# Performance work log

Measured on AMD Instinct MI355X. Metric: run time of the kernel, lower is better.

The kernel has to match this reference:

```python
import jax, jax.numpy as jnp
import numpy as np

B, S, H = 2, 2048, 1024
N_HEAD = 16
HEAD_DIM = H // N_HEAD


def setup_inputs() -> dict:
    key = jax.random.key(0)
    ks = jax.random.split(key, 8)
    init = 0.02
    return {
        "hidden_states": jax.random.normal(ks[0], (B, S, H), dtype=jnp.float32),
        "residual": jax.random.normal(ks[1], (B, S, H), dtype=jnp.float32),
        "alibi": jax.random.normal(ks[2], (B * N_HEAD, 1, S), dtype=jnp.float32),
        "attention_mask": jnp.ones((B, S), dtype=bool),
        "w_qkv": jax.random.normal(ks[3], (H, 3 * H), dtype=jnp.float32) * init,
        "b_qkv": jax.random.normal(ks[4], (3 * H,), dtype=jnp.float32) * init,
        "w_o": jax.random.normal(ks[5], (H, H), dtype=jnp.float32) * init,
        "b_o": jax.random.normal(ks[6], (H,), dtype=jnp.float32) * init,
        "layer_number": 4,
    }


def reference(hidden_states, residual, alibi, attention_mask, w_qkv, b_qkv, w_o, b_o, layer_number):
    b, s, h = hidden_states.shape
    nh, hd = N_HEAD, HEAD_DIM
    # fused QKV projection: (B,S,3H) -> (B,S,nh,3*hd) -> split
    fused_qkv = (hidden_states @ w_qkv + b_qkv).reshape(b, s, nh, 3 * hd)
    query, key, value = jnp.split(fused_qkv, 3, axis=-1)  # each (B,S,nh,hd)

    L = max(int(layer_number), 1)
    alpha = 1.0 / (np.sqrt(hd).astype(np.float32) * L)
    beta = 1.0 / L

    # scores = beta*alibi + alpha * q@k^T, reshaped to (B,nh,Sq,Sk)
    scores = jnp.einsum("bqnh,bknh->bnqk", query, key) * alpha
    scores = scores + beta * alibi.reshape(b, nh, 1, s)
    # FlaxBloomScaledSoftmax applies scale = layer_number before masking
    scores = scores * L

    # fused causal + padding mask (attention_mask_func): keep = causal & pad_q & pad_k
    causal = jnp.tril(jnp.ones((s, s), dtype=bool))
    pad = attention_mask  # (B,S) bool, True = attend
    keep = causal[None, None, :, :] & pad[:, None, :, None] & pad[:, None, None, :]  # (B,1,S,S)

    masked_scores = jnp.where(keep, scores, jnp.float32(-10000.0))
    probs = jax.nn.softmax(masked_scores.astype(jnp.float32), axis=-1) * keep
    probs = probs.astype(hidden_states.dtype)

    context = jnp.einsum("bnqk,bknh->bqnh", probs, value).reshape(b, s, h)
    attn_output = context @ w_o + b_o + residual
    return attn_output
```

## Files before the change

### kernel.cpp

```cpp
#include <hip/hip_runtime.h>
#include <hip/hip_bf16.h>

#define S_LEN 2048
#define HID   1024
#define NHEAD 16
#define HDIM  64
#define NBH   32

#define QSCALE 0.18033688f
#define LOG2E  1.44269504f

typedef __attribute__((ext_vector_type(8))) short short8;
typedef __attribute__((ext_vector_type(4))) float f32x4;

__device__ inline void gload_lds16(const void* g, void* l) {
  __builtin_amdgcn_global_load_lds(
      (const __attribute__((address_space(1))) void*)g,
      (__attribute__((address_space(3))) void*)l, 16, 0, 0);
}

__device__ inline ushort f2bf(float f) {
  __hip_bfloat16 h = __float2bfloat16(f);
  return *reinterpret_cast<const ushort*>(&h);
}

__device__ inline float exp2_fast(float x) {
  float r;
  asm("v_exp_f32 %0, %1" : "=v"(r) : "v"(x));
  return r;
}

__global__ __launch_bounds__(256) void convert_bf16(
    const float* __restrict__ in, ushort* __restrict__ out, int n8)
{
    int i = blockIdx.x * 256 + threadIdx.x;
    if (i < n8) {
        float4 a = ((const float4*)in)[i * 2];
        float4 b = ((const float4*)in)[i * 2 + 1];
        union { ushort u[8]; uint4 v; } o;
        o.u[0]=f2bf(a.x); o.u[1]=f2bf(a.y); o.u[2]=f2bf(a.z); o.u[3]=f2bf(a.w);
        o.u[4]=f2bf(b.x); o.u[5]=f2bf(b.y); o.u[6]=f2bf(b.z); o.u[7]=f2bf(b.w);
        ((uint4*)out)[i] = o.v;
    }
}

__global__ __launch_bounds__(256) void transpose_convert(
    const float* __restrict__ in, ushort* __restrict__ out, int R, int C)
{
    __shared__ ushort Ls[64][72];
    const int c0 = blockIdx.x * 64, r0 = blockIdx.y * 64;
    const int t = threadIdx.x;
    const int tr = t >> 4, tc = (t & 15) * 4;
    #pragma unroll
    for (int i = 0; i < 4; ++i) {
        int gr = r0 + tr + i * 16;
        float4 v = *(const float4*)(in + (size_t)gr * C + c0 + tc);
        Ls[tc + 0][tr + i * 16] = f2bf(v.x);
        Ls[tc + 1][tr + i * 16] = f2bf(v.y);
        Ls[tc + 2][tr + i * 16] = f2bf(v.z);
        Ls[tc + 3][tr + i * 16] = f2bf(v.w);
    }
    __syncthreads();
    #pragma unroll
    for (int i = 0; i < 4; ++i) {
        int oc = c0 + tr + i * 16;
        ushort4 v = *(const ushort4*)&Ls[tr + i * 16][tc];
        *(ushort4*)(out + (size_t)oc * R + r0 + tc) = v;
    }
}

__global__ __launch_bounds__(512, 2) void qkv_gemm_mfma(
    const ushort* __restrict__ A, const ushort* __restrict__ Bt,
    const float* __restrict__ bias,
    ushort* __restrict__ Q, ushort* __restrict__ K, ushort* __restrict__ V)
{
    __shared__ __align__(16) ushort As[2][256 * 64];
    __shared__ __align__(16) ushort Bs[2][192 * 64];
    const int tid = threadIdx.x;
    const int l   = tid & 63;
    const int w   = tid >> 6;
    const int wm  = w >> 2;
    const int wn  = w & 3;
    const int l7  = l & 7, l15 = l & 15, g = l >> 4;
    const int srow = l >> 3;
    const int schunk = l7 ^ srow;

    int lin = blockIdx.y * 16 + blockIdx.x;
    int swz = (lin & 7) * 32 + (lin >> 3);
    const int m0 = (swz >> 4) * 256;
    const int n0 = (swz & 15) * 192;

    f32x4 acc[8][3];
    #pragma unroll
    for (int i = 0; i < 8; ++i)
        #pragma unroll
        for (int j = 0; j < 3; ++j) acc[i][j] = (f32x4){0.f, 0.f, 0.f, 0.f};

#define STG_A(tt, qq) gload_lds16(A + (size_t)(m0 + (qq)*64 + w*8 + srow)*1024 \
                                    + (tt)*64 + schunk*8,                      \
                                  As[(tt) & 1] + ((qq)*64 + w*8)*64)
#define STG_B(tt, qq) gload_lds16(Bt + (size_t)(n0 + (qq)*64 + w*8 + srow)*1024 \
                                    + (tt)*64 + schunk*8,                       \
                                  Bs[(tt) & 1] + ((qq)*64 + w*8)*64)
#define LD_A(bb, mf, kk) (*(const short8*)(As[bb] + ((mf)*32 + wm*16 + l15)*64 \
                                           + ((((kk)*4 + g) ^ l7) << 3)))
#define LD_B(bb, nf, kk) (*(const short8*)(Bs[bb] + (wn*48 + (nf)*16 + l15)*64 \
                                           + ((((kk)*4 + g) ^ l7) << 3)))

    #pragma unroll
    for (int qq = 0; qq < 4; ++qq) STG_A(0, qq);
    #pragma unroll
    for (int qq = 0; qq < 3; ++qq) STG_B(0, qq);
    #pragma unroll
    for (int qq = 0; qq < 3; ++qq) { STG_A(1, qq); STG_B(1, qq); }
    asm volatile("s_waitcnt vmcnt(6)" ::: "memory");
    __builtin_amdgcn_s_barrier();

    short8 bfr[6];

    for (int it = 0; it < 8; ++it) {
        const int t = 2 * it;
        #pragma unroll
        for (int ph = 0; ph < 4; ++ph) {
            short8 afr[4];
            afr[0] = LD_A(0, 2*ph,     0);
            afr[1] = LD_A(0, 2*ph,     1);
            afr[2] = LD_A(0, 2*ph + 1, 0);
            afr[3] = LD_A(0, 2*ph + 1, 1);
            if (ph == 0) {
                #pragma unroll
                for (int nf = 0; nf < 3; ++nf) {
                    bfr[nf*2 + 0] = LD_B(0, nf, 0);
                    bfr[nf*2 + 1] = LD_B(0, nf, 1);
                }
            }
            if (ph == 0) { STG_A(t + 1, 3); }
            else if (t + 2 < 16) { STG_A(t + 2, ph - 1); STG_B(t + 2, ph - 1); }
            __builtin_amdgcn_s_barrier();
            asm volatile("s_waitcnt lgkmcnt(0)" ::: "memory");
            __builtin_amdgcn_sched_barrier(0);
            __builtin_amdgcn_s_setprio(1);
            #pragma unroll
            for (int kk = 0; kk < 2; ++kk)
                #pragma unroll
                for (int mi = 0; mi < 2; ++mi)
                    #pragma unroll
                    for (int nf = 0; nf < 3; ++nf)
                        acc[2*ph + mi][nf] = __builtin_amdgcn_mfma_f32_16x16x32_bf16(
                            afr[mi*2 + kk], bfr[nf*2 + kk], acc[2*ph + mi][nf], 0, 0, 0);
            __builtin_amdgcn_s_setprio(0);
            if (ph == 3) {
                if (it == 7) asm volatile("s_waitcnt vmcnt(0)" ::: "memory");
                else         asm volatile("s_waitcnt vmcnt(6)" ::: "memory");
            }
            __builtin_amdgcn_s_barrier();
        }
        #pragma unroll
        for (int ph = 0; ph < 4; ++ph) {
            short8 afr[4];
            afr[0] = LD_A(1, 2*ph,     0);
            afr[1] = LD_A(1, 2*ph,     1);
            afr[2] = LD_A(1, 2*ph + 1, 0);
            afr[3] = LD_A(1, 2*ph + 1, 1);
            if (ph == 0) {
                #pragma unroll
                for (int nf = 0; nf < 3; ++nf) {
                    bfr[nf*2 + 0] = LD_B(1, nf, 0);
                    bfr[nf*2 + 1] = LD_B(1, nf, 1);
                }
            }
            if (ph == 0) { if (t + 2 < 16) STG_A(t + 2, 3); }
            else if (t + 3 < 16) { STG_A(t + 3, ph - 1); STG_B(t + 3, ph - 1); }
            __builtin_amdgcn_s_barrier();
            asm volatile("s_waitcnt lgkmcnt(0)" ::: "memory");
            __builtin_amdgcn_sched_barrier(0);
            __builtin_amdgcn_s_setprio(1);
            #pragma unroll
            for (int kk = 0; kk < 2; ++kk)
                #pragma unroll
                for (int mi = 0; mi < 2; ++mi)
                    #pragma unroll
                    for (int nf = 0; nf < 3; ++nf)
                        acc[2*ph + mi][nf] = __builtin_amdgcn_mfma_f32_16x16x32_bf16(
                            afr[mi*2 + kk], bfr[nf*2 + kk], acc[2*ph + mi][nf], 0, 0, 0);
            __builtin_amdgcn_s_setprio(0);
            if (ph == 3) asm volatile("s_waitcnt vmcnt(6)" ::: "memory");
            __builtin_amdgcn_s_barrier();
        }
    }
#undef STG_A
#undef STG_B
#undef LD_A
#undef LD_B

    #pragma unroll
    for (int nf = 0; nf < 3; ++nf) {
        int gcol = n0 + wn * 48 + nf * 16 + l15;
        int head = gcol / 192;
        int rem  = gcol - head * 192;
        int which = rem >> 6;
        int d     = rem & 63;
        float bv = bias[gcol];
        #pragma unroll
        for (int mf = 0; mf < 8; ++mf) {
            int grow = m0 + mf * 32 + wm * 16 + g * 4;
            int bb = grow >> 11;
            int ss = grow & 2047;
            int bhh = (bb << 4) + head;
            if (which == 2) {
                ushort4 pk;
                pk.x = f2bf(acc[mf][nf][0] + bv);
                pk.y = f2bf(acc[mf][nf][1] + bv);
                pk.z = f2bf(acc[mf][nf][2] + bv);
                pk.w = f2bf(acc[mf][nf][3] + bv);
                *(ushort4*)(V + ((size_t)bhh * 64 + d) * S_LEN + ss) = pk;
            } else {
                ushort* plane = (which == 0) ? Q : K;
                float sc = (which == 0) ? QSCALE : 1.0f;
                ushort* dst = plane + (((size_t)bhh * S_LEN + ss) << 6) + d;
                #pragma unroll
                for (int r = 0; r < 4; ++r)
                    dst[(size_t)r << 6] = f2bf((acc[mf][nf][r] + bv) * sc);
            }
        }
    }
}

#define GEMM_STAGE(A_, Bt_, kk0, buf) do {                                    \
    _Pragma("unroll")                                                         \
    for (int i = 0; i < 4; ++i) {                                             \
        int row = i * 32 + w * 8 + srow;                                      \
        gload_lds16(A_ + (size_t)(m0 + row) * 1024 + (kk0) + schunk * 8,      \
                    Asl[buf] + (i * 32 + w * 8) * 64);                        \
        gload_lds16(Bt_ + (size_t)(n0 + row) * 1024 + (kk0) + schunk * 8,     \
                    Bsl[buf] + (i * 32 + w * 8) * 64);                        \
    }                                                                         \
} while (0)

#define GEMM_CORE(A_, Bt_)                                                    \
    __shared__ ushort Asl[2][128 * 64];                                       \
    __shared__ ushort Bsl[2][128 * 64];                                       \
    const int tid = threadIdx.x;                                              \
    const int l = tid & 63;                                                   \
    const int w = tid >> 6;                                                   \
    const int wm = (w >> 1) * 64;                                             \
    const int wn = (w & 1) * 64;                                              \
    const int m0 = blockIdx.y * 128;                                          \
    const int n0 = blockIdx.x * 128;                                          \
    const int l15 = l & 15, g = l >> 4;                                       \
    const int srow = l >> 3;                                                  \
    const int schunk = (l & 7) ^ srow;                                        \
    f32x4 acc[4][4];                                                          \
    _Pragma("unroll")                                                         \
    for (int i = 0; i < 4; ++i)                                               \
        _Pragma("unroll")                                                     \
        for (int j = 0; j < 4; ++j) acc[i][j] = (f32x4){0.f, 0.f, 0.f, 0.f};  \
    GEMM_STAGE(A_, Bt_, 0, 0);                                                \
    __syncthreads();                                                          \
    for (int ks = 0; ks < 16; ++ks) {                                         \
        const int cur = ks & 1;                                               \
        if (ks < 15) GEMM_STAGE(A_, Bt_, (ks + 1) * 64, cur ^ 1);             \
        const ushort* Acur = Asl[cur];                                        \
        const ushort* Bcur = Bsl[cur];                                        \
        _Pragma("unroll")                                                     \
        for (int kk = 0; kk < 2; ++kk) {                                      \
            short8 af[4], bf[4];                                              \
            _Pragma("unroll")                                                 \
            for (int mf = 0; mf < 4; ++mf) {                                  \
                int row = wm + mf * 16 + l15;                                 \
                int ch = (kk * 4 + g) ^ (row & 7);                            \
                af[mf] = *(const short8*)(Acur + row * 64 + ch * 8);          \
            }                                                                 \
            _Pragma("unroll")                                                 \
            for (int nf = 0; nf < 4; ++nf) {                                  \
                int row = wn + nf * 16 + l15;                                 \
                int ch = (kk * 4 + g) ^ (row & 7);                            \
                bf[nf] = *(const short8*)(Bcur + row * 64 + ch * 8);          \
            }                                                                 \
            _Pragma("unroll")                                                 \
            for (int mf = 0; mf < 4; ++mf)                                    \
                _Pragma("unroll")                                             \
                for (int nf = 0; nf < 4; ++nf)                                \
                    acc[mf][nf] = __builtin_amdgcn_mfma_f32_16x16x32_bf16(    \
                        af[mf], bf[nf], acc[mf][nf], 0, 0, 0);                \
        }                                                                     \
        __syncthreads();                                                      \
    }

__global__ __launch_bounds__(256) void out_gemm_mfma(
    const ushort* __restrict__ A, const ushort* __restrict__ Bt,
    const float* __restrict__ bias, const float* __restrict__ resid,
    float* __restrict__ out)
{
    GEMM_CORE(A, Bt)
    #pragma unroll
    for (int nf = 0; nf < 4; ++nf) {
        int gcol = n0 + wn + nf * 16 + l15;
        float bv = bias[gcol];
        #pragma unroll
        for (int mf = 0; mf < 4; ++mf) {
            int grow = m0 + wm + mf * 16 + g * 4;
            #pragma unroll
            for (int r = 0; r < 4; ++r) {
                size_t idx = (size_t)(grow + r) * 1024 + gcol;
                out[idx] = acc[mf][nf][r] + bv + resid[idx];
            }
        }
    }
}

#define STAGE(tt, idx) do {                                                   \
    gload_lds16(Kbh + (size_t)((tt) * 64 + w * 8 + srow) * 64 + schunk * 8,   \
                Ks[idx] + (w * 8) * 64);                                      \
    gload_lds16(Vbh + (size_t)(w * 8 + srow) * S_LEN + (tt) * 64 + schunk * 8,\
                Vs[idx] + (w * 8) * 64);                                      \
} while (0)

#define QK_TILE(SN, tt, idx, FULL) do {                                       \
    const ushort* Kc = Ks[idx];                                               \
    _Pragma("unroll")                                                         \
    for (int kb = 0; kb < 4; ++kb) {                                          \
        float4 a4 = *(const float4*)&alib[(tt) * 64 + kb * 16 + g * 4];       \
        SN[kb] = (f32x4){a4.x, a4.y, a4.z, a4.w};                             \
        if (FULL || (tt) * 64 + kb * 16 <= qmax) {                            \
            int row = kb * 16 + l15;                                          \
            short8 ka0 = *(const short8*)(Kc + row * 64 + ((g ^ l7) << 3));   \
            short8 ka1 = *(const short8*)(Kc + row * 64 + (((4+g) ^ l7) << 3));\
            SN[kb] = __builtin_amdgcn_mfma_f32_16x16x32_bf16(ka0, qb0, SN[kb], 0, 0, 0); \
            SN[kb] = __builtin_amdgcn_mfma_f32_16x16x32_bf16(ka1, qb1, SN[kb], 0, 0, 0); \
        }                                                                     \
    }                                                                         \
} while (0)

#define SM_PV(SC, tt, idx, FULL) do {                                         \
    const ushort* Vc = Vs[idx];                                               \
    ushort* Pw = Ps[w];                                                       \
    float p[16];                                                              \
    _Pragma("unroll")                                                         \
    for (int kb = 0; kb < 4; ++kb) {                                          \
        _Pragma("unroll")                                                     \
        for (int r = 0; r < 4; ++r) {                                         \
            float s = SC[kb][r];                                              \
            if (!FULL) {                                                      \
                int kglob = (tt) * 64 + kb * 16 + g * 4 + r;                  \
                s = (kglob > qglob) ? -1e30f : s;                             \
            }                                                                 \
            p[kb * 4 + r] = s;                                                \
        }                                                                     \
    }                                                                         \
    float mx0 = fmaxf(fmaxf(p[0], p[1]),   fmaxf(p[2], p[3]));                \
    float mx1 = fmaxf(fmaxf(p[4], p[5]),   fmaxf(p[6], p[7]));                \
    float mx2 = fmaxf(fmaxf(p[8], p[9]),   fmaxf(p[10], p[11]));              \
    float mx3 = fmaxf(fmaxf(p[12], p[13]), fmaxf(p[14], p[15]));              \
    float pmax = fmaxf(fmaxf(mx0, mx1), fmaxf(mx2, mx3));                     \
    pmax = fmaxf(pmax, __shfl_xor(pmax, 16));                                 \
    pmax = fmaxf(pmax, __shfl_xor(pmax, 32));                                 \
    if (!__all(pmax <= m + 11.5415603f)) {          \
        float mn = fmaxf(m, pmax);                                            \
        float resc = exp2_fast(m - mn);                                       \
        m = mn; lsum *= resc;                                                 \
        _Pragma("unroll")                                                     \
        for (int nb = 0; nb < 4; ++nb) oacc[nb] *= resc;                      \
    }                                                                         \
    _Pragma("unroll")                                                         \
    for (int i = 0; i < 16; ++i) p[i] = exp2_fast(p[i] - m);                  \
    float sm0 = (p[0] + p[1]) + (p[2] + p[3]);                                \
    float sm1 = (p[4] + p[5]) + (p[6] + p[7]);                                \
    float sm2 = (p[8] + p[9]) + (p[10] + p[11]);                              \
    float sm3 = (p[12] + p[13]) + (p[14] + p[15]);                            \
    float rsum = (sm0 + sm1) + (sm2 + sm3);                                   \
    rsum += __shfl_xor(rsum, 16);                                             \
    rsum += __shfl_xor(rsum, 32);                                             \
    lsum += rsum;                                                             \
    _Pragma("unroll")                                                         \
    for (int kb = 0; kb < 4; ++kb) {                                          \
        ushort4 pk;                                                           \
        pk.x = f2bf(p[kb * 4 + 0]); pk.y = f2bf(p[kb * 4 + 1]);               \
        pk.z = f2bf(p[kb * 4 + 2]); pk.w = f2bf(p[kb * 4 + 3]);               \
        int chunk = kb * 2 + (g >> 1);                                        \
        *(ushort4*)(Pw + l15 * 64 + ((chunk ^ l7) << 3) + ((g & 1) << 2)) = pk;\
    }                                                                         \
    short8 pb0 = *(const short8*)(Pw + l15 * 64 + ((g ^ l7) << 3));           \
    short8 pb1 = *(const short8*)(Pw + l15 * 64 + (((4 + g) ^ l7) << 3));     \
    _Pragma("unroll")                                                         \
    for (int nb = 0; nb < 4; ++nb) {                                          \
        int row = nb * 16 + l15;                                              \
        short8 va0 = *(const short8*)(Vc + row * 64 + ((g ^ l7) << 3));       \
        oacc[nb] = __builtin_amdgcn_mfma_f32_16x16x32_bf16(va0, pb0, oacc[nb], 0, 0, 0); \
    }                                                                         \
    if (FULL || (tt) * 64 + 32 <= qmax) {                                     \
        _Pragma("unroll")                                                     \
        for (int nb = 0; nb < 4; ++nb) {                                      \
            int row = nb * 16 + l15;                                          \
            short8 va1 = *(const short8*)(Vc + row * 64 + (((4 + g) ^ l7) << 3)); \
            oacc[nb] = __builtin_amdgcn_mfma_f32_16x16x32_bf16(va1, pb1, oacc[nb], 0, 0, 0); \
        }                                                                     \
    }                                                                         \
} while (0)

__global__ __launch_bounds__(512, 4) void attn_mfma(
    const ushort* __restrict__ Qp, const ushort* __restrict__ Kp,
    const ushort* __restrict__ Vtp, const float* __restrict__ alibi,
    ushort* __restrict__ ctx)
{
    __shared__ ushort Ks[3][64 * 64];
    __shared__ ushort Vs[3][64 * 64];
    __shared__ ushort Ps[8][16 * 64];
    __shared__ __align__(16) float alib[S_LEN];

    const int bh  = blockIdx.y;
    const int qt  = (blockIdx.y & 16) ? (int)blockIdx.x : 15 - (int)blockIdx.x;
    const int tid = threadIdx.x;
    const int w   = tid >> 6;
    const int l   = tid & 63;
    const int l7  = l & 7, l15 = l & 15, g = l >> 4;
    const int q0  = qt * 128;

    const ushort* Qbh = Qp  + (size_t)bh * S_LEN * HDIM;
    const ushort* Kbh = Kp  + (size_t)bh * S_LEN * HDIM;
    const ushort* Vbh = Vtp + (size_t)bh * HDIM * S_LEN;
    const float*  abh = alibi + (size_t)bh * S_LEN;

    const int qglob = q0 + w * 16 + l15;
    const int qmax  = q0 + w * 16 + 15;
    const int qmin  = q0 + w * 16;

    short8 qb0 = *(const short8*)(Qbh + (size_t)qglob * 64 + g * 8);
    short8 qb1 = *(const short8*)(Qbh + (size_t)qglob * 64 + 32 + g * 8);

    float m = -1e30f, lsum = 0.f;
    f32x4 oacc[4];
    #pragma unroll
    for (int nb = 0; nb < 4; ++nb) oacc[nb] = (f32x4){0.f, 0.f, 0.f, 0.f};

    const int srow   = l >> 3;
    const int schunk = (l & 7) ^ srow;

    {
        float4 a = *(const float4*)(abh + tid * 4);
        a.x *= LOG2E; a.y *= LOG2E; a.z *= LOG2E; a.w *= LOG2E;
        *(float4*)(alib + tid * 4) = a;
    }
    STAGE(0, 0);
    __syncthreads();
    STAGE(1, 1);

    f32x4 sa[4], sb[4];
    QK_TILE(sa, 0, 0, 0);

    const int nt = 2 * qt + 2;
    int ipv = 0, iqk = 1, ist = 2;
    for (int t = 0; t < nt; t += 2) {
        __syncthreads();
        if (t + 2 < nt) STAGE(t + 2, ist);
        if ((t + 1 < nt) && ((t + 1) * 64 + 63 <= qmin)) {
            QK_TILE(sb, t + 1, iqk, 1);
            SM_PV(sa, t, ipv, 1);
        } else {
            if ((t + 1 < nt) && ((t + 1) * 64 <= qmax)) QK_TILE(sb, t + 1, iqk, 0);
            if (t * 64 <= qmax) SM_PV(sa, t, ipv, 0);
        }
        { int tmp = ipv; ipv = iqk; iqk = ist; ist = tmp; }

        __syncthreads();
        if (t + 3 < nt) STAGE(t + 3, ist);
        if ((t + 2 < nt) && ((t + 2) * 64 + 63 <= qmin)) {
            QK_TILE(sa, t + 2, iqk, 1);
            SM_PV(sb, t + 1, ipv, 1);
        } else {
            if ((t + 2 < nt) && ((t + 2) * 64 <= qmax)) QK_TILE(sa, t + 2, iqk, 0);
            if ((t + 1) * 64 <= qmax) SM_PV(sb, t + 1, ipv, 0);
        }
        { int tmp = ipv; ipv = iqk; iqk = ist; ist = tmp; }
    }

    const int bb = bh >> 4, hh = bh & 15;
    float inv = 1.0f / lsum;
    ushort* crow = ctx + (size_t)(bb * S_LEN + qglob) * 1024 + hh * 64;
    #pragma unroll
    for (int nb = 0; nb < 4; ++nb) {
        ushort4 pk;
        pk.x = f2bf(oacc[nb][0] * inv);
        pk.y = f2bf(oacc[nb][1] * inv);
        pk.z = f2bf(oacc[nb][2] * inv);
        pk.w = f2bf(oacc[nb][3] * inv);
        *(ushort4*)(crow + nb * 16 + g * 4) = pk;
    }
}

extern "C" void kernel_launch(void* const* d_in, const int* in_sizes, int n_in,
                              void* d_out, int out_size, void* d_ws, size_t ws_size,
                              hipStream_t stream) {
    const float* X      = (const float*)d_in[0];
    const float* resid  = (const float*)d_in[1];
    const float* alibi  = (const float*)d_in[2];
    const float* w_qkv  = (const float*)d_in[4];
    const float* b_qkv  = (const float*)d_in[5];
    const float* w_o    = (const float*)d_in[6];
    const float* b_o    = (const float*)d_in[7];

    const size_t plane = (size_t)NBH * S_LEN * HDIM;
    ushort* Xb   = (ushort*)d_ws;
    ushort* Wqkt = Xb + (size_t)4096 * 1024;
    ushort* Wot  = Wqkt + (size_t)3072 * 1024;
    ushort* Qb   = Wot + (size_t)1024 * 1024;
    ushort* Kb   = Qb + plane;
    ushort* Vbt  = Qb + 2 * plane;
    ushort* ctx  = Qb + 3 * plane;
    float*  out  = (float*)d_out;

    convert_bf16<<<2048, 256, 0, stream>>>(X, Xb, 4096 * 1024 / 8);
    dim3 gt1(3072 / 64, 1024 / 64);
    transpose_convert<<<gt1, 256, 0, stream>>>(w_qkv, Wqkt, 1024, 3072);
    dim3 gt2(1024 / 64, 1024 / 64);
    transpose_convert<<<gt2, 256, 0, stream>>>(w_o, Wot, 1024, 1024);

    dim3 g1(3072 / 192, 4096 / 256);
    qkv_gemm_mfma<<<g1, 512, 0, stream>>>(Xb, Wqkt, b_qkv, Qb, Kb, Vbt);

    dim3 g2(S_LEN / 128, NBH);
    attn_mfma<<<g2, 512, 0, stream>>>(Qb, Kb, Vbt, alibi, ctx);

    dim3 g3(1024 / 128, 4096 / 128);
    out_gemm_mfma<<<g3, 256, 0, stream>>>(ctx, Wot, b_o, resid, out);
}
```

Baseline: 121.6 us.

## Split attention KV range into two blocks per query tile and combine partials

Each query tile's causal key range is split in half across two blocks, split-K style. Each block writes an unnormalized bf16 partial output plus its running max and sum, and a new combine kernel merges the two partials with log-sum-exp weights. The aim is to double the number of attention blocks and cut the longest per-block serial loop, improving load balance and occupancy. In exchange it adds an extra kernel launch, extra global traffic for the partials, and an extra bf16 rounding of the unnormalized partial outputs. It also reuses the Xb and Wqkt workspace buffers as scratch.

```diff
diff --git a/kernel.cpp b/kernel.cpp
--- a/kernel.cpp
+++ b/kernel.cpp
@@ -22,6 +22,10 @@
 __device__ inline ushort f2bf(float f) {
   __hip_bfloat16 h = __float2bfloat16(f);
   return *reinterpret_cast<const ushort*>(&h);
+}
+
+__device__ inline float bf2f(ushort u) {
+  union { uint i; float f; } v; v.i = ((uint)u) << 16; return v.f;
 }
 
 __device__ inline float exp2_fast(float x) {
@@ -363,7 +367,7 @@
         for (int nb = 0; nb < 4; ++nb) oacc[nb] *= resc;                      \
     }                                                                         \
     _Pragma("unroll")                                                         \
-    for (int i = 0; i < 16; ++i) p[i] = exp2_fast(p[i] - m);                  \
+    for (int i = 0; i < 16; ++i) { p[i] = exp2_fast(p[i] - m); }              \
     float sm0 = (p[0] + p[1]) + (p[2] + p[3]);                                \
     float sm1 = (p[4] + p[5]) + (p[6] + p[7]);                                \
     float sm2 = (p[8] + p[9]) + (p[10] + p[11]);                              \
@@ -401,21 +405,26 @@
 __global__ __launch_bounds__(512, 4) void attn_mfma(
     const ushort* __restrict__ Qp, const ushort* __restrict__ Kp,
     const ushort* __restrict__ Vtp, const float* __restrict__ alibi,
-    ushort* __restrict__ ctx)
+    ushort* __restrict__ part0, ushort* __restrict__ ctx,
+    float2* __restrict__ ml)
 {
     __shared__ ushort Ks[3][64 * 64];
     __shared__ ushort Vs[3][64 * 64];
     __shared__ ushort Ps[8][16 * 64];
     __shared__ __align__(16) float alib[S_LEN];
 
-    const int bh  = blockIdx.y;
-    const int qt  = (blockIdx.y & 16) ? (int)blockIdx.x : 15 - (int)blockIdx.x;
+    const int bh    = blockIdx.y;
+    const int qt    = 15 - ((int)blockIdx.x >> 1);
+    const int split = blockIdx.x & 1;
     const int tid = threadIdx.x;
     const int w   = tid >> 6;
     const int l   = tid & 63;
     const int l7  = l & 7, l15 = l & 15, g = l >> 4;
     const int q0  = qt * 128;
 
+    const int t0 = split ? (qt + 1) : 0;
+    const int t1 = split ? (2 * qt + 2) : (qt + 1);
+
     const ushort* Qbh = Qp  + (size_t)bh * S_LEN * HDIM;
     const ushort* Kbh = Kp  + (size_t)bh * S_LEN * HDIM;
     const ushort* Vbh = Vtp + (size_t)bh * HDIM * S_LEN;
@@ -441,51 +450,80 @@
         a.x *= LOG2E; a.y *= LOG2E; a.z *= LOG2E; a.w *= LOG2E;
         *(float4*)(alib + tid * 4) = a;
     }
-    STAGE(0, 0);
+    STAGE(t0, 0);
     __syncthreads();
-    STAGE(1, 1);
+    if (t0 + 1 < t1) STAGE(t0 + 1, 1);
 
     f32x4 sa[4], sb[4];
-    QK_TILE(sa, 0, 0, 0);
-
-    const int nt = 2 * qt + 2;
+    QK_TILE(sa, t0, 0, 0);
+
     int ipv = 0, iqk = 1, ist = 2;
-    for (int t = 0; t < nt; t += 2) {
+    for (int t = t0; t < t1; t += 2) {
         __syncthreads();
-        if (t + 2 < nt) STAGE(t + 2, ist);
-        if ((t + 1 < nt) && ((t + 1) * 64 + 63 <= qmin)) {
+        if (t + 2 < t1) STAGE(t + 2, ist);
+        if ((t + 1 < t1) && ((t + 1) * 64 + 63 <= qmin)) {
             QK_TILE(sb, t + 1, iqk, 1);
             SM_PV(sa, t, ipv, 1);
         } else {
-            if ((t + 1 < nt) && ((t + 1) * 64 <= qmax)) QK_TILE(sb, t + 1, iqk, 0);
+            if ((t + 1 < t1) && ((t + 1) * 64 <= qmax)) QK_TILE(sb, t + 1, iqk, 0);
             if (t * 64 <= qmax) SM_PV(sa, t, ipv, 0);
         }
         { int tmp = ipv; ipv = iqk; iqk = ist; ist = tmp; }
 
         __syncthreads();
-        if (t + 3 < nt) STAGE(t + 3, ist);
-        if ((t + 2 < nt) && ((t + 2) * 64 + 63 <= qmin)) {
+        if (t + 3 < t1) STAGE(t + 3, ist);
+        if ((t + 2 < t1) && ((t + 2) * 64 + 63 <= qmin)) {
             QK_TILE(sa, t + 2, iqk, 1);
             SM_PV(sb, t + 1, ipv, 1);
         } else {
-            if ((t + 2 < nt) && ((t + 2) * 64 <= qmax)) QK_TILE(sa, t + 2, iqk, 0);
-            if ((t + 1) * 64 <= qmax) SM_PV(sb, t + 1, ipv, 0);
+            if ((t + 2 < t1) && ((t + 2) * 64 <= qmax)) QK_TILE(sa, t + 2, iqk, 0);
+            if ((t + 1 < t1) && ((t + 1) * 64 <= qmax)) SM_PV(sb, t + 1, ipv, 0);
         }
         { int tmp = ipv; ipv = iqk; iqk = ist; ist = tmp; }
     }
 
     const int bb = bh >> 4, hh = bh & 15;
-    float inv = 1.0f / lsum;
-    ushort* crow = ctx + (size_t)(bb * S_LEN + qglob) * 1024 + hh * 64;
+    ushort* obase = split ? ctx : part0;
+    ushort* crow = obase + (size_t)(bb * S_LEN + qglob) * 1024 + hh * 64;
     #pragma unroll
     for (int nb = 0; nb < 4; ++nb) {
         ushort4 pk;
-        pk.x = f2bf(oacc[nb][0] * inv);
-        pk.y = f2bf(oacc[nb][1] * inv);
-        pk.z = f2bf(oacc[nb][2] * inv);
-        pk.w = f2bf(oacc[nb][3] * inv);
+        pk.x = f2bf(oacc[nb][0]);
+        pk.y = f2bf(oacc[nb][1]);
+        pk.z = f2bf(oacc[nb][2]);
+        pk.w = f2bf(oacc[nb][3]);
         *(ushort4*)(crow + nb * 16 + g * 4) = pk;
     }
+    if (g == 0)
+        ml[((size_t)split * NBH + bh) * S_LEN + qglob] = make_float2(m, lsum);
+}
+
+__global__ __launch_bounds__(256) void attn_combine(
+    const ushort* __restrict__ p0, ushort* __restrict__ ctx,
+    const float2* __restrict__ ml)
+{
+    const int bh = blockIdx.y;
+    const int qg = blockIdx.x;
+    const int t  = threadIdx.x;
+    const int qloc = t >> 4, dp = t & 15;
+    const int q  = qg * 16 + qloc;
+    const int bb = bh >> 4, hh = bh & 15;
+    const size_t base = (size_t)(bb * S_LEN + q) * 1024 + hh * 64 + dp * 4;
+    float2 a = ml[(size_t)bh * S_LEN + q];
+    float2 c = ml[(size_t)(NBH + bh) * S_LEN + q];
+    float ms = fmaxf(a.x, c.x);
+    float w0 = exp2_fast(a.x - ms);
+    float w1 = exp2_fast(c.x - ms);
+    float inv = 1.0f / (a.y * w0 + c.y * w1);
+    w0 *= inv; w1 *= inv;
+    ushort4 o0 = *(const ushort4*)(p0 + base);
+    ushort4 o1 = *(const ushort4*)(ctx + base);
+    ushort4 r;
+    r.x = f2bf(bf2f(o0.x) * w0 + bf2f(o1.x) * w1);
+    r.y = f2bf(bf2f(o0.y) * w0 + bf2f(o1.y) * w1);
+    r.z = f2bf(bf2f(o0.z) * w0 + bf2f(o1.z) * w1);
+    r.w = f2bf(bf2f(o0.w) * w0 + bf2f(o1.w) * w1);
+    *(ushort4*)(ctx + base) = r;
 }
 
 extern "C" void kernel_launch(void* const* d_in, const int* in_sizes, int n_in,
@@ -507,6 +545,8 @@
     ushort* Kb   = Qb + plane;
     ushort* Vbt  = Qb + 2 * plane;
     ushort* ctx  = Qb + 3 * plane;
+    ushort* part0 = Xb;
+    float2* ml    = (float2*)Wqkt;
     float*  out  = (float*)d_out;
 
     convert_bf16<<<2048, 256, 0, stream>>>(X, Xb, 4096 * 1024 / 8);
@@ -518,8 +558,11 @@
     dim3 g1(3072 / 192, 4096 / 256);
     qkv_gemm_mfma<<<g1, 512, 0, stream>>>(Xb, Wqkt, b_qkv, Qb, Kb, Vbt);
 
-    dim3 g2(S_LEN / 128, NBH);
-    attn_mfma<<<g2, 512, 0, stream>>>(Qb, Kb, Vbt, alibi, ctx);
+    dim3 g2(32, NBH);
+    attn_mfma<<<g2, 512, 0, stream>>>(Qb, Kb, Vbt, alibi, part0, ctx, ml);
+
+    dim3 gc(S_LEN / 16, NBH);
+    attn_combine<<<gc, 256, 0, stream>>>(part0, ctx, ml);
 
     dim3 g3(1024 / 128, 4096 / 128);
     out_gemm_mfma<<<g3, 256, 0, stream>>>(ctx, Wot, b_o, resid, out);
```

After: 143.0 us. 17.6% more time.
